# Kernel tuning notes

Measured on AMD Instinct MI355X. Metric: run time of the kernel, lower is better.

Reference implementation:

```python
import jax, jax.numpy as jnp
import numpy as np
import math

MODEL_DIM = 1024
HEAD_DIM = 64
NUM_HEADS = 16
FF_MULT = 4
FF_DIM = FF_MULT * MODEL_DIM
ATTN_DIM = NUM_HEADS * HEAD_DIM
FUSED_DIMS = (ATTN_DIM, ATTN_DIM, ATTN_DIM, FF_DIM, FF_DIM)


def setup_inputs() -> dict:
    key = jax.random.key(0)
    k_x, k_in, k_attn, k_ff = jax.random.split(key, 4)
    B, S = 2, 2048
    inputs = jax.random.normal(k_x, (B, S, MODEL_DIM), dtype=jnp.float32)
    # LayerNorm affine params (torch defaults: weight=1, bias=0)
    ln_w = jnp.ones((MODEL_DIM,), dtype=jnp.float32)
    ln_b = jnp.zeros((MODEL_DIM,), dtype=jnp.float32)
    # Linear weights stored as [in, out] (equivalent to torch W.T)
    s_in = 1.0 / math.sqrt(MODEL_DIM)
    w_in = jax.random.uniform(k_in, (MODEL_DIM, sum(FUSED_DIMS)), jnp.float32, -s_in, s_in)
    s_a = 1.0 / math.sqrt(ATTN_DIM)
    w_attn = jax.random.uniform(k_attn, (ATTN_DIM, MODEL_DIM), jnp.float32, -s_a, s_a)
    s_f = 1.0 / math.sqrt(FF_DIM)
    w_ff = jax.random.uniform(k_ff, (FF_DIM, MODEL_DIM), jnp.float32, -s_f, s_f)
    return {"inputs": inputs, "ln_w": ln_w, "ln_b": ln_b,
            "w_in": w_in, "w_attn": w_attn, "w_ff": w_ff}


def _layer_norm(x, w, b, eps=1e-5):
    mu = jnp.mean(x, axis=-1, keepdims=True)
    var = jnp.var(x, axis=-1, keepdims=True)
    return (x - mu) * jax.lax.rsqrt(var + eps) * w + b


def reference(inputs, ln_w, ln_b, w_in, w_attn, w_ff):
    B, S, D = inputs.shape
    units = _layer_norm(inputs, ln_w, ln_b)
    proj = units @ w_in                                   # [B,S,3*A+2*F]
    splits = np.cumsum(FUSED_DIMS)[:-1]
    q, k, v, ff, ff_gate = jnp.split(proj, splits, axis=-1)
    # split heads: [B,S,H*d] -> [B,H,S,d]
    def heads(t):
        return t.reshape(B, S, NUM_HEADS, HEAD_DIM).transpose(0, 2, 1, 3)
    q, k, v = heads(q), heads(k), heads(v)
    scale = 1.0 / math.sqrt(HEAD_DIM)
    score = jnp.einsum('bhsd,bhTd->bhsT', q, k) * scale   # [B,H,S,S]
    weight = jax.nn.softmax(score, axis=-1)
    attn = jnp.einsum('bhsT,bhTd->bhsd', weight, v)       # [B,H,S,d]
    concat = attn.transpose(0, 2, 1, 3).reshape(B, S, ATTN_DIM)
    attn_out = concat @ w_attn                            # [B,S,D]
    ff_out = (ff * jax.nn.gelu(ff_gate, approximate=True)) @ w_ff
    return inputs + attn_out + ff_out
```

## Files before the change

### kernel.cpp

```cpp
#include <hip/hip_runtime.h>
#include <hip/hip_bf16.h>
#include <cstdint>
#include <cstddef>

typedef __bf16 bf16;
typedef __bf16 bf16x8 __attribute__((ext_vector_type(8)));
typedef float f32x4 __attribute__((ext_vector_type(4)));

#define MFMA16(a, b, c) __builtin_amdgcn_mfma_f32_16x16x32_bf16(a, b, c, 0, 0, 0)

#define GLOBAL_LOAD_LDS16(gptr, lptr)                                          \
  __builtin_amdgcn_global_load_lds(                                            \
      (const __attribute__((address_space(1))) void*)(gptr),                   \
      (__attribute__((address_space(3))) void*)(lptr), 16, 0, 0)

__global__ __launch_bounds__(256) void prep(const float* __restrict__ w_in,
                                            const float* __restrict__ w_attn,
                                            const float* __restrict__ w_ff,
                                            bf16* __restrict__ wt_in,
                                            bf16* __restrict__ wtcat,
                                            const float* __restrict__ x,
                                            const float* __restrict__ ln_w,
                                            const float* __restrict__ ln_b,
                                            bf16* __restrict__ xn) {
  __shared__ __align__(16) float t[64][65];
  const int tid = threadIdx.x;
  if (blockIdx.x < 4096) {
    int id = blockIdx.x;
    const float* src; bf16* dst;
    int srcN, n0, k0, kcol0;
    size_t LDO;
    bool win;
    if (id < 2816) {
      src = w_in; dst = wt_in; srcN = 11264; LDO = 1024;
      n0 = (id % 176) * 64; k0 = (id / 176) * 64; kcol0 = 0; win = true;
    } else if (id < 3072) {
      id -= 2816; src = w_attn; dst = wtcat; srcN = 1024; LDO = 5120;
      n0 = (id % 16) * 64; k0 = (id / 16) * 64; kcol0 = 0; win = false;
    } else {
      id -= 3072; src = w_ff; dst = wtcat; srcN = 1024; LDO = 5120;
      n0 = (id % 16) * 64; k0 = (id / 16) * 64; kcol0 = 1024; win = false;
    }
    int drow0;
    if (!win || n0 < 3072) {
      drow0 = n0;
    } else if (n0 < 7168) {
      int m = n0 - 3072; drow0 = 3072 + ((m >> 6) << 7);
    } else {
      int m = n0 - 7168; drow0 = 3072 + ((m >> 6) << 7) + 64;
    }
#pragma unroll
    for (int i = 0; i < 16; i++) {
      int k = i * 4 + (tid >> 6), n = tid & 63;
      t[k][n] = src[(size_t)(k0 + k) * srcN + n0 + n];
    }
    __syncthreads();
#pragma unroll
    for (int j = 0; j < 2; j++) {
      int n = j * 32 + (tid >> 3), kc = (tid & 7) * 8;
      bf16x8 o;
#pragma unroll
      for (int u = 0; u < 8; u++) o[u] = (bf16)t[kc + u][n];
      *(bf16x8*)&dst[(size_t)(drow0 + n) * LDO + kcol0 + k0 + kc] = o;
    }
  } else {
    __shared__ float rs[256], rss[256];
    const int row = blockIdx.x - 4096;
    const float* xr = x + (size_t)row * 1024;
    float4 v = *(const float4*)&xr[tid * 4];
    float s = v.x + v.y + v.z + v.w;
    float ss = v.x * v.x + v.y * v.y + v.z * v.z + v.w * v.w;
    rs[tid] = s; rss[tid] = ss;
    __syncthreads();
    for (int off = 128; off > 0; off >>= 1) {
      if (tid < off) { rs[tid] += rs[tid + off]; rss[tid] += rss[tid + off]; }
      __syncthreads();
    }
    const float mean = rs[0] * (1.f / 1024.f);
    const float var = rss[0] * (1.f / 1024.f) - mean * mean;
    const float rstd = rsqrtf(var + 1e-5f);
    const float* vp = (const float*)&v;
    for (int i = 0; i < 4; i++) {
      int c = tid * 4 + i;
      xn[(size_t)row * 1024 + c] = (bf16)((vp[i] - mean) * rstd * ln_w[c] + ln_b[c]);
    }
  }
}

__global__ __launch_bounds__(256) void flash_attn(const bf16* __restrict__ proj,
                                                  const bf16* __restrict__ vt,
                                                  bf16* __restrict__ hcat) {
  __shared__ __align__(16) char smem[50176];
  bf16* Ks = (bf16*)smem;
  bf16* Vs = (bf16*)(smem + 16384);
  bf16* Ps = (bf16*)(smem + 32768);
  const int tid = threadIdx.x;
  const int wave = tid >> 6, lane = tid & 63;
  const int quad = lane >> 4, l16 = lane & 15;
  const int q0 = blockIdx.x * 64;
  const int h = blockIdx.y, b = blockIdx.z;
  constexpr size_t LDP = 3072;
  const bf16* Qb = proj + (size_t)b * 2048 * LDP + h * 64;
  const bf16* Kb = proj + (size_t)b * 2048 * LDP + 1024 + h * 64;
  const bf16* Vt = vt + (size_t)(b * 16 + h) * 64 * 2048;

  const int qrow = q0 + wave * 16 + l16;
  bf16x8 aq0r = *(const bf16x8*)&Qb[(size_t)qrow * LDP + quad * 8];
  bf16x8 aq1r = *(const bf16x8*)&Qb[(size_t)qrow * LDP + 32 + quad * 8];
  bf16x8 aq0, aq1;
#pragma unroll
  for (int i = 0; i < 8; i++) {
    aq0[i] = (bf16)((float)aq0r[i] * 0.125f);
    aq1[i] = (bf16)((float)aq1r[i] * 0.125f);
  }

  f32x4 O[4] = {};
  float plrow[4] = {0.f, 0.f, 0.f, 0.f};

  const int krow_ = wave * 8 + (lane >> 3);
  const int kq_ = ((lane & 7) ^ (krow_ & 7)) * 8;
  const int vrow_ = wave * 4 + (lane >> 4);
  const int vq_ = ((lane & 15) ^ (vrow_ & 15)) * 8;

  for (int j0 = 0; j0 < 2048; j0 += 128) {
#pragma unroll
    for (int p = 0; p < 4; p++) {
      int kr = p * 32 + krow_;
      GLOBAL_LOAD_LDS16(&Kb[(size_t)(j0 + kr) * LDP + kq_],
                        &Ks[kr * 64 + (lane & 7) * 8]);
      int vr = p * 16 + vrow_;
      GLOBAL_LOAD_LDS16(&Vt[(size_t)vr * 2048 + j0 + vq_],
                        &Vs[vr * 128 + (lane & 15) * 8]);
    }
    __syncthreads();

    f32x4 sa[8];
#pragma unroll
    for (int nt = 0; nt < 8; nt++) {
      int r = nt * 16 + l16;
      bf16x8 bk0 = *(const bf16x8*)&Ks[r * 64 + (quad ^ (r & 7)) * 8];
      bf16x8 bk1 = *(const bf16x8*)&Ks[r * 64 + ((quad + 4) ^ (r & 7)) * 8];
      f32x4 t = {};
      t = MFMA16(aq0, bk0, t);
      sa[nt] = MFMA16(aq1, bk1, t);
    }

    bf16* Pw = Ps + wave * (16 * 136);
#pragma unroll
    for (int r = 0; r < 4; r++) {
      bf16* pr = &Pw[(quad * 4 + r) * 136];
      float ts = 0.f;
#pragma unroll
      for (int nt = 0; nt < 8; nt++) {
        float p = __expf(sa[nt][r]);
        pr[nt * 16 + l16] = (bf16)p;
        ts += p;
      }
      plrow[r] += ts;
    }

#pragma unroll
    for (int kg = 0; kg < 4; kg++) {
      bf16x8 aP = *(const bf16x8*)&Pw[l16 * 136 + kg * 32 + quad * 8];
#pragma unroll
      for (int nb = 0; nb < 4; nb++) {
        int vrr = nb * 16 + l16;
        int vsl = ((kg * 4 + quad) ^ (vrr & 15)) * 8;
        bf16x8 bv = *(const bf16x8*)&Vs[vrr * 128 + vsl];
        O[nb] = MFMA16(aP, bv, O[nb]);
      }
    }
    __syncthreads();
  }

#pragma unroll
  for (int r = 0; r < 4; r++) {
    float ts = plrow[r];
#pragma unroll
    for (int d = 1; d < 16; d <<= 1) ts += __shfl_xor(ts, d, 64);
    float inv = 1.f / ts;
    size_t row = (size_t)b * 2048 + q0 + wave * 16 + quad * 4 + r;
#pragma unroll
    for (int nb = 0; nb < 4; nb++)
      hcat[row * 5120 + h * 64 + nb * 16 + l16] = (bf16)(O[nb][r] * inv);
  }
}

__global__ __launch_bounds__(512, 2) void gemm_proj(const bf16* __restrict__ A,
                                                    const bf16* __restrict__ Bt,
                                                    bf16* __restrict__ proj,
                                                    bf16* __restrict__ hcat,
                                                    bf16* __restrict__ vt) {
  constexpr int K = 1024, NT = 32;
  __shared__ __align__(16) char smem[131072];
  const int tid = threadIdx.x;
  const int wave = tid >> 6, lane = tid & 63;
  const int quad = lane >> 4, l16 = lane & 15;
  const int wm0 = (wave >> 2) * 128, wn0 = (wave & 3) * 64;
  const size_t rowA0 = (size_t)blockIdx.y * 256;
  const size_t rowB0 = (size_t)blockIdx.x * 256;
  const bf16* Ag = A + rowA0 * K;
  const bf16* Bg = Bt + rowB0 * K;

  const int srow = tid >> 2;
  const int sslot = tid & 3;
  const int rslot = (quad ^ ((l16 >> 1) & 3)) * 8;

  f32x4 acc[8][4] = {};

  auto STAGE = [&](int kt, int buf) {
    bf16* As = (bf16*)(smem + buf * 32768);
    bf16* Bs = As + 256 * 32;
    const int k0 = kt * 32;
#pragma unroll
    for (int p = 0; p < 2; p++) {
      int r = p * 128 + srow;
      int kq = (sslot ^ ((r >> 1) & 3)) * 8;
      GLOBAL_LOAD_LDS16(&Ag[(size_t)r * K + k0 + kq], &As[r * 32 + sslot * 8]);
      GLOBAL_LOAD_LDS16(&Bg[(size_t)r * K + k0 + kq], &Bs[r * 32 + sslot * 8]);
    }
  };

  STAGE(0, 0);
  STAGE(1, 1);
  STAGE(2, 2);
  asm volatile("s_waitcnt vmcnt(8)" ::: "memory");
  __builtin_amdgcn_s_barrier();
  asm volatile("" ::: "memory");

#pragma unroll 1
  for (int kt = 0; kt < NT; kt++) {
    if (kt + 3 < NT) STAGE(kt + 3, (kt + 3) & 3);
    const bf16* As = (const bf16*)(smem + (kt & 3) * 32768);
    const bf16* Bs = As + 256 * 32;
    bf16x8 bfr[4];
#pragma unroll
    for (int j = 0; j < 4; j++)
      bfr[j] = *(const bf16x8*)&Bs[(wn0 + j * 16 + l16) * 32 + rslot];
#pragma unroll
    for (int ih = 0; ih < 2; ih++) {
      bf16x8 af[4];
#pragma unroll
      for (int i = 0; i < 4; i++)
        af[i] = *(const bf16x8*)&As[(wm0 + (ih * 4 + i) * 16 + l16) * 32 + rslot];
      __builtin_amdgcn_s_setprio(1);
#pragma unroll
      for (int i = 0; i < 4; i++)
#pragma unroll
        for (int j = 0; j < 4; j++)
          acc[ih * 4 + i][j] = MFMA16(af[i], bfr[j], acc[ih * 4 + i][j]);
      __builtin_amdgcn_s_setprio(0);
    }
    if (kt < NT - 3) {
      asm volatile("s_waitcnt vmcnt(8)" ::: "memory");
    } else if (kt == NT - 3) {
      asm volatile("s_waitcnt vmcnt(4)" ::: "memory");
    } else {
      asm volatile("s_waitcnt vmcnt(0)" ::: "memory");
    }
    __builtin_amdgcn_s_barrier();
    asm volatile("" ::: "memory");
  }

  {
    const int xb = (int)blockIdx.x;
    const int T2 = xb - 12;
    bf16* Cs = (bf16*)smem;
    constexpr int LDC2 = 264;
#pragma unroll 1
    for (int h = 0; h < 2; h++) {
      if ((wave >> 2) == h) {
#pragma unroll
        for (int i = 0; i < 8; i++)
#pragma unroll
          for (int j = 0; j < 4; j++)
#pragma unroll
            for (int r = 0; r < 4; r++)
              Cs[(i * 16 + quad * 4 + r) * LDC2 + wn0 + j * 16 + l16] =
                  (bf16)acc[i][j][r];
      }
      __syncthreads();
      if (xb < 8) {
#pragma unroll
        for (int it = 0; it < 8; it++) {
          int idx = it * 512 + tid;
          int row = idx >> 5, ch = (idx & 31) * 8;
          *(bf16x8*)&proj[(rowA0 + h * 128 + row) * 3072 + rowB0 + ch] =
              *(const bf16x8*)&Cs[row * LDC2 + ch];
        }
      } else if (T2 < 0) {
        const int g0 = (int)rowA0 + h * 128;
        const int bb = g0 >> 11, sloc0 = g0 & 2047;
        const int hb = (xb - 8) * 4;
        bf16* vtb = vt + ((size_t)(bb * 16 + hb) * 64) * 2048 + sloc0;
#pragma unroll
        for (int it = 0; it < 8; it++) {
          int u = it * 512 + tid;
          int col = u & 255, sc = u >> 8;
          bf16x8 o;
#pragma unroll
          for (int k = 0; k < 8; k++) o[k] = Cs[(sc * 8 + k) * LDC2 + col];
          *(bf16x8*)&vtb[(size_t)col * 2048 + sc * 8] = o;
        }
      } else {
#pragma unroll
        for (int it = 0; it < 4; it++) {
          int idx = it * 512 + tid;
          int row = idx >> 4;
          int p = (idx >> 3) & 1, c8 = (idx & 7) * 8;
          bf16x8 f = *(const bf16x8*)&Cs[row * LDC2 + p * 128 + c8];
          bf16x8 g = *(const bf16x8*)&Cs[row * LDC2 + p * 128 + 64 + c8];
          bf16x8 o;
#pragma unroll
          for (int i = 0; i < 8; i++) {
            float xg = (float)g[i];
            float u = 0.7978845608f * (xg + 0.044715f * xg * xg * xg);
            float gl = xg / (1.f + __expf(-2.f * u));
            o[i] = (bf16)((float)f[i] * gl);
          }
          *(bf16x8*)&hcat[(rowA0 + h * 128 + row) * 5120 + 1024 +
                          (2 * T2 + p) * 64 + c8] = o;
        }
      }
      __syncthreads();
    }
  }
}

__global__ __launch_bounds__(256) void gemm_out(const bf16* __restrict__ A,
                                                const bf16* __restrict__ Bt,
                                                bf16* __restrict__ part) {
  constexpr int LDAB = 5120, LDC = 136;
  __shared__ __align__(16) char smem[32768];
  bf16* As = (bf16*)smem;
  bf16* Bs = As + 128 * 64;
  bf16* Cs = (bf16*)smem;
  const int tid = threadIdx.x;
  const int wave = tid >> 6, lane = tid & 63;
  const int quad = lane >> 4, l16 = lane & 15;
  constexpr int NM = 4, NN = 4;
  const int wm0 = (wave >> 1) * 64, wn0 = (wave & 1) * 64;
  const size_t rowA0 = (size_t)blockIdx.y * 128;
  const size_t rowB0 = (size_t)blockIdx.x * 128;
  const int kbeg = blockIdx.z * 1280, kend = kbeg + 1280;

  const int srow = tid >> 3;
  const int sq = ((tid & 7) ^ (srow & 7)) * 8;
  const int sslot = (tid & 7) * 8;

  f32x4 acc[NM][NN] = {};

  for (int k0 = kbeg; k0 < kend; k0 += 64) {
#pragma unroll
    for (int p = 0; p < 4; p++) {
      int r = p * 32 + srow;
      GLOBAL_LOAD_LDS16(&A[(rowA0 + r) * LDAB + k0 + sq], &As[r * 64 + sslot]);
      GLOBAL_LOAD_LDS16(&Bt[(rowB0 + r) * LDAB + k0 + sq], &Bs[r * 64 + sslot]);
    }
    __syncthreads();
#pragma unroll
    for (int c = 0; c < 2; c++) {
      bf16x8 af[NM], bfr[NN];
#pragma unroll
      for (int i = 0; i < NM; i++) {
        int r = wm0 + i * 16 + l16;
        af[i] = *(const bf16x8*)&As[r * 64 + ((c * 4 + quad) ^ (r & 7)) * 8];
      }
#pragma unroll
      for (int j = 0; j < NN; j++) {
        int r = wn0 + j * 16 + l16;
        bfr[j] = *(const bf16x8*)&Bs[r * 64 + ((c * 4 + quad) ^ (r & 7)) * 8];
      }
#pragma unroll
      for (int i = 0; i < NM; i++)
#pragma unroll
        for (int j = 0; j < NN; j++)
          acc[i][j] = MFMA16(af[i], bfr[j], acc[i][j]);
    }
    __syncthreads();
  }

  bf16* dst = part + (size_t)blockIdx.z * (4096 * 1024);
#pragma unroll
  for (int half = 0; half < 2; half++) {
    if ((wave >> 1) == half) {
#pragma unroll
      for (int i = 0; i < NM; i++)
#pragma unroll
        for (int j = 0; j < NN; j++)
#pragma unroll
          for (int r = 0; r < 4; r++)
            Cs[(i * 16 + quad * 4 + r) * LDC + wn0 + j * 16 + l16] =
                (bf16)acc[i][j][r];
    }
    __syncthreads();
    const int c0 = (tid & 15) * 8;
#pragma unroll
    for (int it = 0; it < 4; it++) {
      int row = (tid >> 4) + it * 16;
      *(bf16x8*)&dst[(rowA0 + half * 64 + row) * 1024 + rowB0 + c0] =
          *(const bf16x8*)&Cs[row * LDC + c0];
    }
    __syncthreads();
  }
}

__global__ __launch_bounds__(256) void reduce_out(const float* __restrict__ x,
                                                  const bf16* __restrict__ part,
                                                  float* __restrict__ out) {
  const size_t i = ((size_t)blockIdx.x * 256 + threadIdx.x) * 8;
  constexpr size_t SL = 4096 * 1024;
  float r[8];
  float4 x0 = *(const float4*)&x[i];
  float4 x1 = *(const float4*)&x[i + 4];
  r[0] = x0.x; r[1] = x0.y; r[2] = x0.z; r[3] = x0.w;
  r[4] = x1.x; r[5] = x1.y; r[6] = x1.z; r[7] = x1.w;
#pragma unroll
  for (int z = 0; z < 4; z++) {
    bf16x8 p = *(const bf16x8*)&part[z * SL + i];
#pragma unroll
    for (int k = 0; k < 8; k++) r[k] += (float)p[k];
  }
  float4 o0 = {r[0], r[1], r[2], r[3]};
  float4 o1 = {r[4], r[5], r[6], r[7]};
  *(float4*)&out[i] = o0;
  *(float4*)&out[i + 4] = o1;
}

extern "C" void kernel_launch(void* const* d_in, const int* in_sizes, int n_in,
                              void* d_out, int out_size, void* d_ws, size_t ws_size,
                              hipStream_t stream) {
  const float* x      = (const float*)d_in[0];
  const float* ln_w   = (const float*)d_in[1];
  const float* ln_b   = (const float*)d_in[2];
  const float* w_in   = (const float*)d_in[3];
  const float* w_attn = (const float*)d_in[4];
  const float* w_ff   = (const float*)d_in[5];
  float* out = (float*)d_out;
  char* ws = (char*)d_ws;

  bf16* wt_in = (bf16*)(ws);
  bf16* wtcat = (bf16*)(ws + 23068672);
  bf16* xn    = (bf16*)(ws + 33554432);
  bf16* proj  = (bf16*)(ws + 41943040);
  bf16* part  = (bf16*)(ws + 67108864);
  bf16* vt    = (bf16*)(ws + 100663296);
  bf16* hcat  = (bf16*)(ws + 134217728);

  prep<<<8192, 256, 0, stream>>>(w_in, w_attn, w_ff, wt_in, wtcat,
                                 x, ln_w, ln_b, xn);
  gemm_proj<<<dim3(44, 16), 512, 0, stream>>>(xn, wt_in, proj, hcat, vt);
  flash_attn<<<dim3(32, 16, 2), 256, 0, stream>>>(proj, vt, hcat);
  gemm_out<<<dim3(8, 32, 4), 256, 0, stream>>>(hcat, wtcat, part);
  reduce_out<<<2048, 256, 0, stream>>>(x, part, out);
}
```

Before: 378.4 us.

## Cut gemm_proj LDS to triple-buffer and rewrite gemm_out as 256x256 pipelined tile

gemm_proj drops from a 4-stage to a 3-stage global_load_lds ring, shrinking LDS from 128KB to 96KB so two 512-thread blocks can share a CU under launch_bounds(512,2). gemm_out is rebuilt on the same design: 256x256 tiles, 8 waves, a 3-buffer async prefetch pipeline with swizzled LDS, split-K of 4, and a grid of 4x16x4 instead of 8x32x4. The aim is more data reuse per block and hiding global latency in the output GEMM. The trade-off is fewer blocks (256) in gemm_out and shallower prefetch in gemm_proj.

```diff
diff --git a/kernel.cpp b/kernel.cpp
--- a/kernel.cpp
+++ b/kernel.cpp
@@ -192,7 +192,7 @@
                                                     bf16* __restrict__ hcat,
                                                     bf16* __restrict__ vt) {
   constexpr int K = 1024, NT = 32;
-  __shared__ __align__(16) char smem[131072];
+  __shared__ __align__(16) char smem[98304];
   const int tid = threadIdx.x;
   const int wave = tid >> 6, lane = tid & 63;
   const int quad = lane >> 4, l16 = lane & 15;
@@ -223,15 +223,15 @@
 
   STAGE(0, 0);
   STAGE(1, 1);
-  STAGE(2, 2);
-  asm volatile("s_waitcnt vmcnt(8)" ::: "memory");
+  asm volatile("s_waitcnt vmcnt(4)" ::: "memory");
   __builtin_amdgcn_s_barrier();
   asm volatile("" ::: "memory");
 
+  int cbuf = 0, sbuf = 2;
 #pragma unroll 1
   for (int kt = 0; kt < NT; kt++) {
-    if (kt + 3 < NT) STAGE(kt + 3, (kt + 3) & 3);
-    const bf16* As = (const bf16*)(smem + (kt & 3) * 32768);
+    if (kt + 2 < NT) STAGE(kt + 2, sbuf);
+    const bf16* As = (const bf16*)(smem + cbuf * 32768);
     const bf16* Bs = As + 256 * 32;
     bf16x8 bfr[4];
 #pragma unroll
@@ -251,15 +251,15 @@
           acc[ih * 4 + i][j] = MFMA16(af[i], bfr[j], acc[ih * 4 + i][j]);
       __builtin_amdgcn_s_setprio(0);
     }
-    if (kt < NT - 3) {
-      asm volatile("s_waitcnt vmcnt(8)" ::: "memory");
-    } else if (kt == NT - 3) {
+    if (kt + 2 < NT) {
       asm volatile("s_waitcnt vmcnt(4)" ::: "memory");
     } else {
       asm volatile("s_waitcnt vmcnt(0)" ::: "memory");
     }
     __builtin_amdgcn_s_barrier();
     asm volatile("" ::: "memory");
+    cbuf = (cbuf == 2) ? 0 : cbuf + 1;
+    sbuf = (sbuf == 2) ? 0 : sbuf + 1;
   }
 
   {
@@ -327,81 +327,107 @@
   }
 }
 
-__global__ __launch_bounds__(256) void gemm_out(const bf16* __restrict__ A,
-                                                const bf16* __restrict__ Bt,
-                                                bf16* __restrict__ part) {
-  constexpr int LDAB = 5120, LDC = 136;
-  __shared__ __align__(16) char smem[32768];
-  bf16* As = (bf16*)smem;
-  bf16* Bs = As + 128 * 64;
-  bf16* Cs = (bf16*)smem;
+__global__ __launch_bounds__(512, 2) void gemm_out(const bf16* __restrict__ A,
+                                                   const bf16* __restrict__ Bt,
+                                                   bf16* __restrict__ part) {
+  constexpr int LDAB = 5120, NT = 40;
+  __shared__ __align__(16) char smem[98304];
   const int tid = threadIdx.x;
   const int wave = tid >> 6, lane = tid & 63;
   const int quad = lane >> 4, l16 = lane & 15;
-  constexpr int NM = 4, NN = 4;
-  const int wm0 = (wave >> 1) * 64, wn0 = (wave & 1) * 64;
-  const size_t rowA0 = (size_t)blockIdx.y * 128;
-  const size_t rowB0 = (size_t)blockIdx.x * 128;
-  const int kbeg = blockIdx.z * 1280, kend = kbeg + 1280;
-
-  const int srow = tid >> 3;
-  const int sq = ((tid & 7) ^ (srow & 7)) * 8;
-  const int sslot = (tid & 7) * 8;
-
-  f32x4 acc[NM][NN] = {};
-
-  for (int k0 = kbeg; k0 < kend; k0 += 64) {
-#pragma unroll
-    for (int p = 0; p < 4; p++) {
-      int r = p * 32 + srow;
-      GLOBAL_LOAD_LDS16(&A[(rowA0 + r) * LDAB + k0 + sq], &As[r * 64 + sslot]);
-      GLOBAL_LOAD_LDS16(&Bt[(rowB0 + r) * LDAB + k0 + sq], &Bs[r * 64 + sslot]);
-    }
-    __syncthreads();
-#pragma unroll
-    for (int c = 0; c < 2; c++) {
-      bf16x8 af[NM], bfr[NN];
-#pragma unroll
-      for (int i = 0; i < NM; i++) {
-        int r = wm0 + i * 16 + l16;
-        af[i] = *(const bf16x8*)&As[r * 64 + ((c * 4 + quad) ^ (r & 7)) * 8];
-      }
-#pragma unroll
-      for (int j = 0; j < NN; j++) {
-        int r = wn0 + j * 16 + l16;
-        bfr[j] = *(const bf16x8*)&Bs[r * 64 + ((c * 4 + quad) ^ (r & 7)) * 8];
-      }
-#pragma unroll
-      for (int i = 0; i < NM; i++)
-#pragma unroll
-        for (int j = 0; j < NN; j++)
-          acc[i][j] = MFMA16(af[i], bfr[j], acc[i][j]);
-    }
-    __syncthreads();
-  }
-
-  bf16* dst = part + (size_t)blockIdx.z * (4096 * 1024);
-#pragma unroll
-  for (int half = 0; half < 2; half++) {
-    if ((wave >> 1) == half) {
-#pragma unroll
-      for (int i = 0; i < NM; i++)
-#pragma unroll
-        for (int j = 0; j < NN; j++)
-#pragma unroll
-          for (int r = 0; r < 4; r++)
-            Cs[(i * 16 + quad * 4 + r) * LDC + wn0 + j * 16 + l16] =
-                (bf16)acc[i][j][r];
-    }
-    __syncthreads();
-    const int c0 = (tid & 15) * 8;
-#pragma unroll
-    for (int it = 0; it < 4; it++) {
-      int row = (tid >> 4) + it * 16;
-      *(bf16x8*)&dst[(rowA0 + half * 64 + row) * 1024 + rowB0 + c0] =
-          *(const bf16x8*)&Cs[row * LDC + c0];
-    }
-    __syncthreads();
+  const int wm0 = (wave >> 2) * 128, wn0 = (wave & 3) * 64;
+  const size_t rowA0 = (size_t)blockIdx.y * 256;
+  const size_t rowB0 = (size_t)blockIdx.x * 256;
+  const int kbeg = blockIdx.z * 1280;
+  const bf16* Ag = A + rowA0 * LDAB + kbeg;
+  const bf16* Bg = Bt + rowB0 * LDAB + kbeg;
+
+  const int srow = tid >> 2;
+  const int sslot = tid & 3;
+  const int rslot = (quad ^ ((l16 >> 1) & 3)) * 8;
+
+  f32x4 acc[8][4] = {};
+
+  auto STAGE = [&](int kt, int buf) {
+    bf16* As = (bf16*)(smem + buf * 32768);
+    bf16* Bs = As + 256 * 32;
+    const int k0 = kt * 32;
+#pragma unroll
+    for (int p = 0; p < 2; p++) {
+      int r = p * 128 + srow;
+      int kq = (sslot ^ ((r >> 1) & 3)) * 8;
+      GLOBAL_LOAD_LDS16(&Ag[(size_t)r * LDAB + k0 + kq], &As[r * 32 + sslot * 8]);
+      GLOBAL_LOAD_LDS16(&Bg[(size_t)r * LDAB + k0 + kq], &Bs[r * 32 + sslot * 8]);
+    }
+  };
+
+  STAGE(0, 0);
+  STAGE(1, 1);
+  asm volatile("s_waitcnt vmcnt(4)" ::: "memory");
+  __builtin_amdgcn_s_barrier();
+  asm volatile("" ::: "memory");
+
+  int cbuf = 0, sbuf = 2;
+#pragma unroll 1
+  for (int kt = 0; kt < NT; kt++) {
+    if (kt + 2 < NT) STAGE(kt + 2, sbuf);
+    const bf16* As = (const bf16*)(smem + cbuf * 32768);
+    const bf16* Bs = As + 256 * 32;
+    bf16x8 bfr[4];
+#pragma unroll
+    for (int j = 0; j < 4; j++)
+      bfr[j] = *(const bf16x8*)&Bs[(wn0 + j * 16 + l16) * 32 + rslot];
+#pragma unroll
+    for (int ih = 0; ih < 2; ih++) {
+      bf16x8 af[4];
+#pragma unroll
+      for (int i = 0; i < 4; i++)
+        af[i] = *(const bf16x8*)&As[(wm0 + (ih * 4 + i) * 16 + l16) * 32 + rslot];
+      __builtin_amdgcn_s_setprio(1);
+#pragma unroll
+      for (int i = 0; i < 4; i++)
+#pragma unroll
+        for (int j = 0; j < 4; j++)
+          acc[ih * 4 + i][j] = MFMA16(af[i], bfr[j], acc[ih * 4 + i][j]);
+      __builtin_amdgcn_s_setprio(0);
+    }
+    if (kt + 2 < NT) {
+      asm volatile("s_waitcnt vmcnt(4)" ::: "memory");
+    } else {
+      asm volatile("s_waitcnt vmcnt(0)" ::: "memory");
+    }
+    __builtin_amdgcn_s_barrier();
+    asm volatile("" ::: "memory");
+    cbuf = (cbuf == 2) ? 0 : cbuf + 1;
+    sbuf = (sbuf == 2) ? 0 : sbuf + 1;
+  }
+
+  {
+    bf16* dst = part + (size_t)blockIdx.z * (4096 * 1024);
+    bf16* Cs = (bf16*)smem;
+    constexpr int LDC2 = 264;
+#pragma unroll 1
+    for (int h = 0; h < 2; h++) {
+      if ((wave >> 2) == h) {
+#pragma unroll
+        for (int i = 0; i < 8; i++)
+#pragma unroll
+          for (int j = 0; j < 4; j++)
+#pragma unroll
+            for (int r = 0; r < 4; r++)
+              Cs[(i * 16 + quad * 4 + r) * LDC2 + wn0 + j * 16 + l16] =
+                  (bf16)acc[i][j][r];
+      }
+      __syncthreads();
+#pragma unroll
+      for (int it = 0; it < 8; it++) {
+        int idx = it * 512 + tid;
+        int row = idx >> 5, ch = (idx & 31) * 8;
+        *(bf16x8*)&dst[(rowA0 + h * 128 + row) * 1024 + rowB0 + ch] =
+            *(const bf16x8*)&Cs[row * LDC2 + ch];
+      }
+      __syncthreads();
+    }
   }
 }
 
@@ -451,6 +477,6 @@
                                  x, ln_w, ln_b, xn);
   gemm_proj<<<dim3(44, 16), 512, 0, stream>>>(xn, wt_in, proj, hcat, vt);
   flash_attn<<<dim3(32, 16, 2), 256, 0, stream>>>(proj, vt, hcat);
-  gemm_out<<<dim3(8, 32, 4), 256, 0, stream>>>(hcat, wtcat, part);
+  gemm_out<<<dim3(4, 16, 4), 512, 0, stream>>>(hcat, wtcat, part);
   reduce_out<<<2048, 256, 0, stream>>>(x, part, out);
 }
```

Measured after the change: 354.0 us. 1.07x faster.
